# Optimization experiments

Hardware: AMD Instinct MI355X
Metric: run time of the kernel (lower is better)

## Reference

```python
import jax, jax.numpy as jnp
import numpy as np

NUM_HEADS = 12
DIM = 768
HW = 64                # h = w = 64, seqlen = 4096
L = HW * HW
HIDDEN = 4 * DIM


def _dwconv(img, w, b):
    # img: (C, H, W); w: (C, 1, 3, 3) depthwise; b: (C,)
    y = jax.lax.conv_general_dilated(
        img[None], w, window_strides=(1, 1), padding=((1, 1), (1, 1)),
        feature_group_count=img.shape[0],
        dimension_numbers=('NCHW', 'OIHW', 'NCHW'))[0]
    return y + b[:, None, None]


def _ln(t, w, b, eps=1e-5):
    mu = t.mean(-1, keepdims=True)
    var = ((t - mu) ** 2).mean(-1, keepdims=True)
    return (t - mu) / jnp.sqrt(var + eps) * w + b


def _rope_cos_sin(H, W, D, base=10000.0):
    # MLLA-style axial 2D RoPE over feature dim D: k_max = D // (2*ndim)
    k_max = D // 4
    theta = 1.0 / (base ** (jnp.arange(k_max, dtype=jnp.float32) / k_max))
    ax = jnp.arange(H, dtype=jnp.float32)[:, None, None] * theta  # (H,1,k)
    ay = jnp.arange(W, dtype=jnp.float32)[None, :, None] * theta  # (1,W,k)
    angles = jnp.concatenate([
        jnp.broadcast_to(ax, (H, W, k_max)),
        jnp.broadcast_to(ay, (H, W, k_max))], axis=-1)  # (H, W, D/2)
    return jnp.cos(angles), jnp.sin(angles)


def _rope_apply(t, cos, sin):
    # t: (H, W, D); rotate consecutive feature pairs (complex mult)
    H, W, D = t.shape
    t2 = t.reshape(H, W, D // 2, 2)
    x0, x1 = t2[..., 0], t2[..., 1]
    return jnp.stack([x0 * cos - x1 * sin, x0 * sin + x1 * cos], axis=-1).reshape(H, W, D)


def setup_inputs() -> dict:
    key = jax.random.key(0)
    ks = jax.random.split(key, 18)
    s = 0.02
    f32 = jnp.float32
    return {
        'x': jax.random.normal(ks[0], (L, DIM), f32),
        'cpe1_w': jax.random.normal(ks[1], (DIM, 1, 3, 3), f32) * s,
        'cpe1_b': jnp.zeros((DIM,), f32),
        'norm1_w': jnp.ones((DIM,), f32),
        'norm1_b': jnp.zeros((DIM,), f32),
        'qk_w': jax.random.normal(ks[2], (2 * DIM, DIM), f32) * s,
        'qk_b': jnp.zeros((2 * DIM,), f32),
        'lepe_w': jax.random.normal(ks[3], (DIM, 1, 3, 3), f32) * s,
        'lepe_b': jnp.zeros((DIM,), f32),
        'cpe2_w': jax.random.normal(ks[4], (DIM, 1, 3, 3), f32) * s,
        'cpe2_b': jnp.zeros((DIM,), f32),
        'norm2_w': jnp.ones((DIM,), f32),
        'norm2_b': jnp.zeros((DIM,), f32),
        'fc1_w': jax.random.normal(ks[5], (HIDDEN, DIM), f32) * s,
        'fc1_b': jnp.zeros((HIDDEN,), f32),
        'fc2_w': jax.random.normal(ks[6], (DIM, HIDDEN), f32) * s,
        'fc2_b': jnp.zeros((DIM,), f32),
    }


def reference(x, cpe1_w, cpe1_b, norm1_w, norm1_b, qk_w, qk_b, lepe_w, lepe_b,
              cpe2_w, cpe2_b, norm2_w, norm2_b, fc1_w, fc1_b, fc2_w, fc2_b):
    n, C = x.shape          # (4096, 768)
    Hh = Ww = HW
    h, d = NUM_HEADS, C // NUM_HEADS

    # --- CPE1 + norm1 ---
    x1 = x + _dwconv(x.T.reshape(C, Hh, Ww), cpe1_w, cpe1_b).reshape(C, n).T
    x1 = _ln(x1, norm1_w, norm1_b)

    # --- LinearAttention (ELU+1 kernel, RoPE, LePE) ---
    qk = x1 @ qk_w.T + qk_b                                   # (n, 2C)
    q = qk[:, :C].reshape(n, h, d).transpose(1, 0, 2)          # (h, n, d)
    k = qk[:, C:].reshape(n, h, d).transpose(1, 0, 2)
    v = x1.reshape(n, h, d).transpose(1, 0, 2)
    q = jax.nn.elu(q) + 1.0
    k = jax.nn.elu(k) + 1.0

    cos, sin = _rope_cos_sin(Hh, Ww, C)
    to2d = lambda t: t.transpose(1, 0, 2).reshape(Hh, Ww, C)
    from2d = lambda t: t.reshape(n, h, d).transpose(1, 0, 2)
    q_rope = from2d(_rope_apply(to2d(q), cos, sin))
    k_rope = from2d(_rope_apply(to2d(k), cos, sin))

    z = 1.0 / (jnp.einsum('hnd,hd->hn', q, k.mean(axis=1)) + 1e-6)
    scale = n ** (-0.5)
    kv = jnp.einsum('hnd,hne->hde', k_rope * scale, v * scale)  # (h, d, d)
    a = jnp.einsum('hnd,hde->hne', q_rope, kv) * z[..., None]   # (h, n, d)
    a = a.transpose(1, 0, 2).reshape(n, C)

    lepe_out = _dwconv(x1.T.reshape(C, Hh, Ww), lepe_w, lepe_b).reshape(C, n).T
    x1 = a + lepe_out

    # --- residual + CPE2 + MLP ---
    x = x + x1
    x = x + _dwconv(x.T.reshape(C, Hh, Ww), cpe2_w, cpe2_b).reshape(C, n).T
    y = _ln(x, norm2_w, norm2_b)
    y = jax.nn.silu(y @ fc1_w.T + fc1_b) @ fc2_w.T + fc2_b
    return x + y
```

## Files before the change

### kernel.cpp

```cpp
#include <hip/hip_runtime.h>
#include <hip/hip_bf16.h>
#include <stdint.h>

#define DIM 768
#define NTOK 4096

typedef __bf16 bf16x8_t __attribute__((ext_vector_type(8)));
typedef float f32x4_t __attribute__((ext_vector_type(4)));
typedef unsigned short u16x8 __attribute__((ext_vector_type(8)));

__device__ __forceinline__ float bf2f(unsigned short u) {
    union { unsigned int i; float f; } v; v.i = ((unsigned int)u) << 16; return v.f;
}
__device__ __forceinline__ unsigned short f2bf(float f) {
    union { float f; unsigned int i; } v; v.f = f;
    unsigned int x = v.i;
    unsigned int r = x + 0x7fffu + ((x >> 16) & 1u);
    return (unsigned short)(r >> 16);
}
__device__ __forceinline__ u16x8 pack8(const float4& a, const float4& b) {
    u16x8 o;
    o[0] = f2bf(a.x); o[1] = f2bf(a.y); o[2] = f2bf(a.z); o[3] = f2bf(a.w);
    o[4] = f2bf(b.x); o[5] = f2bf(b.y); o[6] = f2bf(b.z); o[7] = f2bf(b.w);
    return o;
}

__device__ __forceinline__ void gload_lds16(const void* g, void* l) {
    __builtin_amdgcn_global_load_lds((const __attribute__((address_space(1))) void*)g,
                                     (__attribute__((address_space(3))) void*)l, 16, 0, 0);
}

__global__ __launch_bounds__(256) void prep(
    const float* __restrict__ qkw, const float* __restrict__ fc1w, const float* __restrict__ fc2w,
    unsigned short* __restrict__ oqk, unsigned short* __restrict__ ofc1,
    unsigned short* __restrict__ ofc2, float* __restrict__ zbuf)
{
    const int b = blockIdx.x, t = threadIdx.x;
    const float* src; unsigned short* dst; int rel;
    if (b < 1152)      { src = qkw;  dst = oqk;  rel = b; }
    else if (b < 3456) { src = fc1w; dst = ofc1; rel = b - 1152; }
    else if (b < 5760) { src = fc2w; dst = ofc2; rel = b - 3456; }
    else { zbuf[(b - 5760) * 256 + t] = 0.f; return; }
    int i = rel * 1024 + t * 4;
    float4 v = *(const float4*)&src[i];
    ushort4 o;
    o.x = f2bf(v.x); o.y = f2bf(v.y); o.z = f2bf(v.z); o.w = f2bf(v.w);
    *(ushort4*)&dst[i] = o;
}

template<int DO_LN, int BASE_BF16, int CIN_BF16, int PRE_BF16>
__global__ __launch_bounds__(256) void conv_ln(
    const void* __restrict__ base_, const void* __restrict__ cin_,
    const float* __restrict__ cw, const float* __restrict__ cb,
    const float* __restrict__ lnw, const float* __restrict__ lnb,
    void* __restrict__ pre_out, unsigned short* __restrict__ lnb16_out)
{
    const int n = blockIdx.x;
    const int hh = n >> 6, ww = n & 63;
    const int t = threadIdx.x;
    float s[3];
#pragma unroll
    for (int i = 0; i < 3; i++) {
        int c = t + i * 256;
        float acc = cb[c];
#pragma unroll
        for (int dh = -1; dh <= 1; dh++) {
            int h2 = hh + dh;
            if ((unsigned)h2 < 64u) {
#pragma unroll
                for (int dw = -1; dw <= 1; dw++) {
                    int w2 = ww + dw;
                    if ((unsigned)w2 < 64u) {
                        size_t idx = (size_t)(h2 * 64 + w2) * DIM + c;
                        float cv = CIN_BF16 ? bf2f(((const unsigned short*)cin_)[idx])
                                            : ((const float*)cin_)[idx];
                        acc = fmaf(cv, cw[c * 9 + (dh + 1) * 3 + (dw + 1)], acc);
                    }
                }
            }
        }
        size_t idx = (size_t)n * DIM + c;
        float v = (BASE_BF16 ? bf2f(((const unsigned short*)base_)[idx])
                             : ((const float*)base_)[idx]) + acc;
        s[i] = v;
        if (pre_out) {
            if (PRE_BF16) ((unsigned short*)pre_out)[idx] = f2bf(v);
            else          ((float*)pre_out)[idx] = v;
        }
    }
    if (DO_LN) {
        float s1 = s[0] + s[1] + s[2];
        float s2 = s[0] * s[0] + s[1] * s[1] + s[2] * s[2];
#pragma unroll
        for (int o = 32; o; o >>= 1) { s1 += __shfl_xor(s1, o); s2 += __shfl_xor(s2, o); }
        __shared__ float red[8];
        int w = t >> 6, lane = t & 63;
        if (lane == 0) { red[w * 2] = s1; red[w * 2 + 1] = s2; }
        __syncthreads();
        s1 = red[0] + red[2] + red[4] + red[6];
        s2 = red[1] + red[3] + red[5] + red[7];
        float mean = s1 * (1.f / 768.f);
        float var = s2 * (1.f / 768.f) - mean * mean;
        float rstd = rsqrtf(var + 1e-5f);
#pragma unroll
        for (int i = 0; i < 3; i++) {
            int c = t + i * 256;
            float vn = (s[i] - mean) * rstd * lnw[c] + lnb[c];
            lnb16_out[(size_t)n * DIM + c] = f2bf(vn);
        }
    }
}

template<int BM, int NBX, int PR, int PC, int SILU, int OUTBF16, int ADD, int ADDBF16, int ROPE>
__global__ __launch_bounds__(256, 3) void gemm_bt(
    const unsigned short* __restrict__ A, const unsigned short* __restrict__ B,
    const float* __restrict__ bias, const void* __restrict__ addsrc,
    void* __restrict__ outp,
    unsigned short* __restrict__ qr, unsigned short* __restrict__ krs,
    unsigned short* __restrict__ qpre, float* __restrict__ ksum,
    int N, int K)
{
    constexpr int BN  = 64;
    constexpr int RB  = BM / 4;
    constexpr int MF  = RB / 16;
    constexpr int ACW = BM / 32;
    constexpr int BCW = BN / 32;
    constexpr int XC  = NBX / PC;
    __shared__ __align__(128) unsigned short aL[2][BM * 64];
    __shared__ __align__(128) unsigned short bL[2][BN * 64];

    const int xcd = blockIdx.x & 7, local = blockIdx.x >> 3;
    const int brow = (xcd / XC) * PR + local / PC;
    const int bcol = (xcd % XC) * PC + local % PC;
    const int t = threadIdx.x, w = t >> 6, lane = t & 63;
    const int lr = lane >> 3;
    const int sl = (lane & 7) ^ lr;

    const unsigned short* aSrc[ACW];
#pragma unroll
    for (int i = 0; i < ACW; i++)
        aSrc[i] = A + (size_t)(brow * BM + (w * ACW + i) * 8 + lr) * K + sl * 8;
    const unsigned short* bSrc[BCW];
#pragma unroll
    for (int i = 0; i < BCW; i++)
        bSrc[i] = B + (size_t)(bcol * BN + (w * BCW + i) * 8 + lr) * K + sl * 8;

    f32x4_t acc[MF][4];
#pragma unroll
    for (int m = 0; m < MF; m++)
#pragma unroll
        for (int n = 0; n < 4; n++) acc[m][n] = (f32x4_t){0.f, 0.f, 0.f, 0.f};

#define STAGE(buf, k0) do { \
    _Pragma("unroll") for (int i_ = 0; i_ < ACW; i_++) \
        gload_lds16(aSrc[i_] + (k0), &aL[buf][(w * ACW + i_) * 512]); \
    _Pragma("unroll") for (int i_ = 0; i_ < BCW; i_++) \
        gload_lds16(bSrc[i_] + (k0), &bL[buf][(w * BCW + i_) * 512]); } while (0)

    const int nt = K >> 6;
    STAGE(0, 0);
    __syncthreads();

    const int fr = lane & 15;
    const int xr = (fr & 7) << 4;
    const int cbase = (lane >> 4) << 4;
    for (int tt = 0; tt < nt; ++tt) {
        if (tt + 1 < nt) STAGE((tt + 1) & 1, (tt + 1) * 64);
        const char* ab = (const char*)aL[tt & 1];
        const char* bb = (const char*)bL[tt & 1];
#pragma unroll
        for (int ks = 0; ks < 2; ks++) {
            bf16x8_t af[MF], bfv[4];
#pragma unroll
            for (int m = 0; m < MF; m++)
                af[m] = *(const bf16x8_t*)(ab + (((w * RB + m * 16 + fr) * 128 + cbase + ks * 64) ^ xr));
#pragma unroll
            for (int n = 0; n < 4; n++)
                bfv[n] = *(const bf16x8_t*)(bb + (((n * 16 + fr) * 128 + cbase + ks * 64) ^ xr));
            __builtin_amdgcn_s_setprio(1);
#pragma unroll
            for (int m = 0; m < MF; m++)
#pragma unroll
                for (int n = 0; n < 4; n++)
                    acc[m][n] = __builtin_amdgcn_mfma_f32_16x16x32_bf16(af[m], bfv[n], acc[m][n], 0, 0, 0);
            __builtin_amdgcn_s_setprio(0);
        }
        __syncthreads();
    }
#undef STAGE

    const int rb = brow * BM + w * RB + (lane >> 4) * 4;
    const int cb = bcol * BN + fr;

    if constexpr (ROPE) {
        const bool isq = (bcol < 12);
        const bool use_h = ((bcol % 12) < 6);
#pragma unroll
        for (int n = 0; n < 4; n++) {
            int col = cb + n * 16;
            float bs = bias[col];
            int cm = isq ? col : col - 768;
            int p = cm >> 1;
            int pmv = use_h ? p : p - 192;
            float th = __expf(-(float)pmv * (9.210340371976184f / 192.f));
            float kssum = 0.f;
#pragma unroll
            for (int m = 0; m < MF; m++) {
#pragma unroll
                for (int j = 0; j < 4; j++) {
                    int row = rb + m * 16 + j;
                    float v = acc[m][n][j] + bs;
                    float e = v > 0.f ? v + 1.f : __expf(v);
                    float pe = __shfl_xor(e, 1);
                    float pos = use_h ? (float)(row >> 6) : (float)(row & 63);
                    float sa, ca;
                    __sincosf(pos * th, &sa, &ca);
                    float rot = (fr & 1) ? (pe * sa + e * ca) : (e * ca - pe * sa);
                    if (isq) {
                        qr[(size_t)row * 768 + col] = f2bf(rot);
                        qpre[(size_t)row * 768 + col] = f2bf(e);
                    } else {
                        krs[(size_t)row * 768 + cm] = f2bf(rot * 0.015625f);
                        kssum += e;
                    }
                }
            }
            if (!isq) {
                kssum += __shfl_xor(kssum, 16);
                kssum += __shfl_xor(kssum, 32);
                if (lane < 16) atomicAdd(&ksum[cm], kssum);
            }
        }
    } else {
#pragma unroll
        for (int n = 0; n < 4; n++) {
            int col = cb + n * 16;
            float bs = bias ? bias[col] : 0.f;
#pragma unroll
            for (int m = 0; m < MF; m++) {
#pragma unroll
                for (int j = 0; j < 4; j++) {
                    int row = rb + m * 16 + j;
                    float v = acc[m][n][j] + bs;
                    if (SILU) v = v / (1.f + __expf(-v));
                    if (ADD) {
                        size_t idx = (size_t)row * N + col;
                        v += ADDBF16 ? bf2f(((const unsigned short*)addsrc)[idx])
                                     : ((const float*)addsrc)[idx];
                    }
                    if (OUTBF16) ((unsigned short*)outp)[(size_t)row * N + col] = f2bf(v);
                    else ((float*)outp)[(size_t)row * N + col] = v;
                }
            }
        }
    }
}

__global__ __launch_bounds__(256) void kv_accum(
    const unsigned short* __restrict__ krs, const unsigned short* __restrict__ x1b,
    float* __restrict__ kvout)
{
    const int chunk = blockIdx.x, h = blockIdx.y;
    const int n0 = chunk * 128;
    __shared__ float kl[128][64];
    __shared__ float vl[128][64];
    const int t = threadIdx.x;
    const int r = t >> 1, cs = (t & 1) * 32;
#pragma unroll
    for (int j = 0; j < 32; j += 8) {
        u16x8 kk = *(const u16x8*)&krs[(size_t)(n0 + r) * DIM + h * 64 + cs + j];
        u16x8 vv = *(const u16x8*)&x1b[(size_t)(n0 + r) * DIM + h * 64 + cs + j];
#pragma unroll
        for (int e = 0; e < 8; e++) {
            kl[r][cs + j + e] = bf2f(kk[e]);
            vl[r][cs + j + e] = bf2f(vv[e]) * 0.015625f;
        }
    }
    __syncthreads();
    const int td = t >> 4, te = t & 15;
    float a[4][4] = {};
    for (int nn = 0; nn < 128; nn++) {
        f32x4_t kd = *(const f32x4_t*)&kl[nn][td * 4];
        f32x4_t ve = *(const f32x4_t*)&vl[nn][te * 4];
#pragma unroll
        for (int i = 0; i < 4; i++)
#pragma unroll
            for (int j = 0; j < 4; j++)
                a[i][j] = fmaf(kd[i], ve[j], a[i][j]);
    }
#pragma unroll
    for (int i = 0; i < 4; i++)
#pragma unroll
        for (int j = 0; j < 4; j++)
            atomicAdd(&kvout[h * 4096 + (te * 4 + j) * 64 + (td * 4 + i)], a[i][j]);
}

__global__ __launch_bounds__(256) void attn_lepe(
    const unsigned short* __restrict__ qr, const unsigned short* __restrict__ qpre,
    const float* __restrict__ ksum, const float* __restrict__ kvT,
    const float* __restrict__ x, const unsigned short* __restrict__ x1b,
    const float* __restrict__ lepe_w, const float* __restrict__ lepe_b,
    unsigned short* __restrict__ x2b)
{
    const int h = blockIdx.y;
    const int chunk = blockIdx.x;
    const int n0 = chunk * 128;
    const int c0 = h * 64;
    const int R0 = chunk * 2;
    const int t = threadIdx.x, w = t >> 6, lane = t & 63;
    __shared__ __align__(128) unsigned short kvL[64 * 64];
    __shared__ __align__(128) unsigned short x1L[4][64][64];
    __shared__ float zl[128];
    __shared__ float kmL[64];

    {
        const int e = t >> 2, db = (t & 3) * 16;
        const float* src = &kvT[h * 4096 + e * 64 + db];
        float4 v0 = *(const float4*)&src[0];
        float4 v1 = *(const float4*)&src[4];
        float4 v2 = *(const float4*)&src[8];
        float4 v3 = *(const float4*)&src[12];
        int s0 = ((db >> 3) + 0) ^ (e & 7);
        int s1 = ((db >> 3) + 1) ^ (e & 7);
        *(u16x8*)((char*)kvL + e * 128 + s0 * 16) = pack8(v0, v1);
        *(u16x8*)((char*)kvL + e * 128 + s1 * 16) = pack8(v2, v3);
    }
    {
        const int r = t >> 6, ww = t & 63;
        const int rr = R0 - 1 + r;
        const bool ok = (unsigned)rr < 64u;
        const unsigned short* sp = &x1b[(size_t)(rr * 64 + ww) * DIM + c0];
#pragma unroll
        for (int jj = 0; jj < 8; jj++) {
            u16x8 vv;
            if (ok) vv = *(const u16x8*)(sp + jj * 8);
            else    vv = (u16x8)(0);
            *(u16x8*)&x1L[r][ww][jj * 8] = vv;
        }
    }
    if (t < 64) kmL[t] = ksum[h * 64 + t] * (1.f / 4096.f);
    __syncthreads();

    {
        const int tok = t >> 1, half = (t & 1) * 32;
        const unsigned short* qp = &qpre[(size_t)(n0 + tok) * DIM + c0 + half];
        float zs = 0.f;
#pragma unroll
        for (int j = 0; j < 32; j += 8) {
            u16x8 qv = *(const u16x8*)&qp[j];
#pragma unroll
            for (int e = 0; e < 8; e++) zs = fmaf(bf2f(qv[e]), kmL[half + j + e], zs);
        }
        zs += __shfl_xor(zs, 1);
        if ((t & 1) == 0) zl[tok] = 1.f / (zs + 1e-6f);
    }
    __syncthreads();

    const int fr = lane & 15;
    const int kc = (lane >> 4) * 8;
    const unsigned short* qbase = qr + (size_t)(n0 + w * 32 + fr) * DIM + c0 + kc;

    f32x4_t acc[2][4];
#pragma unroll
    for (int m = 0; m < 2; m++)
#pragma unroll
        for (int n = 0; n < 4; n++) acc[m][n] = (f32x4_t){0.f, 0.f, 0.f, 0.f};

#pragma unroll
    for (int ks = 0; ks < 2; ks++) {
        bf16x8_t af[2], bfv[4];
#pragma unroll
        for (int m = 0; m < 2; m++)
            af[m] = *(const bf16x8_t*)(qbase + (size_t)m * 16 * DIM + ks * 32);
#pragma unroll
        for (int n = 0; n < 4; n++) {
            int e = n * 16 + fr;
            int slot = (ks * 4 + (lane >> 4)) ^ (e & 7);
            bfv[n] = *(const bf16x8_t*)((const char*)kvL + e * 128 + slot * 16);
        }
#pragma unroll
        for (int m = 0; m < 2; m++)
#pragma unroll
            for (int n = 0; n < 4; n++)
                acc[m][n] = __builtin_amdgcn_mfma_f32_16x16x32_bf16(af[m], bfv[n], acc[m][n], 0, 0, 0);
    }

    const int r4 = (lane >> 4) * 4;
#pragma unroll
    for (int n = 0; n < 4; n++) {
        const int cc = n * 16 + fr;
        const int c = c0 + cc;
        float w9[9];
#pragma unroll
        for (int q2 = 0; q2 < 9; q2++) w9[q2] = lepe_w[c * 9 + q2];
        const float lb = lepe_b[c];
#pragma unroll
        for (int m = 0; m < 2; m++) {
#pragma unroll
            for (int j = 0; j < 4; j++) {
                const int tr = w * 32 + m * 16 + r4 + j;
                float av = acc[m][n][j] * zl[tr];
                const int ww = tr & 63;
                const int rbase = (tr >> 6) + 1;
                float conv = 0.f;
#pragma unroll
                for (int dh = -1; dh <= 1; dh++) {
#pragma unroll
                    for (int dw = -1; dw <= 1; dw++) {
                        int w2 = ww + dw;
                        if ((unsigned)w2 < 64u)
                            conv = fmaf(bf2f(x1L[rbase + dh][w2][cc]),
                                        w9[(dh + 1) * 3 + (dw + 1)], conv);
                    }
                }
                float xr2 = x[(size_t)(n0 + tr) * DIM + c];
                x2b[(size_t)(n0 + tr) * DIM + c] = f2bf(xr2 + av + conv + lb);
            }
        }
    }
}

extern "C" void kernel_launch(void* const* d_in, const int* in_sizes, int n_in,
                              void* d_out, int out_size, void* d_ws, size_t ws_size,
                              hipStream_t stream) {
    (void)in_sizes; (void)n_in; (void)out_size; (void)ws_size;
    const float* x       = (const float*)d_in[0];
    const float* cpe1_w  = (const float*)d_in[1];
    const float* cpe1_b  = (const float*)d_in[2];
    const float* norm1_w = (const float*)d_in[3];
    const float* norm1_b = (const float*)d_in[4];
    const float* qk_w    = (const float*)d_in[5];
    const float* qk_b    = (const float*)d_in[6];
    const float* lepe_w  = (const float*)d_in[7];
    const float* lepe_b  = (const float*)d_in[8];
    const float* cpe2_w  = (const float*)d_in[9];
    const float* cpe2_b  = (const float*)d_in[10];
    const float* norm2_w = (const float*)d_in[11];
    const float* norm2_b = (const float*)d_in[12];
    const float* fc1_w   = (const float*)d_in[13];
    const float* fc1_b   = (const float*)d_in[14];
    const float* fc2_w   = (const float*)d_in[15];
    const float* fc2_b   = (const float*)d_in[16];
    char* ws = (char*)d_ws;

    constexpr size_t o_qkwb  = 0;
    constexpr size_t o_fc1wb = o_qkwb  + (size_t)1536 * 768 * 2;
    constexpr size_t o_fc2wb = o_fc1wb + (size_t)3072 * 768 * 2;
    constexpr size_t o_x1b   = o_fc2wb + (size_t)768 * 3072 * 2;
    constexpr size_t o_big   = o_x1b   + (size_t)4096 * 768 * 2;
    constexpr size_t o_qr    = o_big   + (size_t)4096 * 3072 * 2;
    constexpr size_t o_krs   = o_qr    + (size_t)4096 * 768 * 2;
    constexpr size_t o_qpre  = o_krs   + (size_t)4096 * 768 * 2;
    constexpr size_t o_ksum  = o_qpre  + (size_t)4096 * 768 * 2;
    constexpr size_t o_kv    = o_ksum  + (size_t)768 * 4;
    constexpr size_t o_x3b   = o_kv    + (size_t)12 * 64 * 64 * 4;
    constexpr size_t o_yb    = o_x3b   + (size_t)4096 * 768 * 2;

    unsigned short* x2b = (unsigned short*)(ws + o_big);
    unsigned short* h_b = (unsigned short*)(ws + o_big);

    prep<<<5955, 256, 0, stream>>>(qk_w, fc1_w, fc2_w,
                                   (unsigned short*)(ws + o_qkwb), (unsigned short*)(ws + o_fc1wb),
                                   (unsigned short*)(ws + o_fc2wb), (float*)(ws + o_ksum));
    conv_ln<1, 0, 0, 0><<<4096, 256, 0, stream>>>(x, x, cpe1_w, cpe1_b, norm1_w, norm1_b,
                                                  nullptr, (unsigned short*)(ws + o_x1b));
    gemm_bt<128, 24, 8, 12, 0, 0, 0, 0, 1><<<768, 256, 0, stream>>>(
        (const unsigned short*)(ws + o_x1b), (const unsigned short*)(ws + o_qkwb),
        qk_b, nullptr, nullptr,
        (unsigned short*)(ws + o_qr), (unsigned short*)(ws + o_krs),
        (unsigned short*)(ws + o_qpre), (float*)(ws + o_ksum),
        1536, 768);
    kv_accum<<<dim3(32, 12), 256, 0, stream>>>((const unsigned short*)(ws + o_krs),
                                               (const unsigned short*)(ws + o_x1b),
                                               (float*)(ws + o_kv));
    attn_lepe<<<dim3(32, 12), 256, 0, stream>>>((const unsigned short*)(ws + o_qr),
                                                (const unsigned short*)(ws + o_qpre),
                                                (const float*)(ws + o_ksum), (const float*)(ws + o_kv),
                                                x, (const unsigned short*)(ws + o_x1b),
                                                lepe_w, lepe_b, x2b);
    conv_ln<1, 1, 1, 1><<<4096, 256, 0, stream>>>(x2b, x2b, cpe2_w, cpe2_b, norm2_w, norm2_b,
                                                  (void*)(ws + o_x3b), (unsigned short*)(ws + o_yb));
    gemm_bt<128, 48, 16, 12, 1, 1, 0, 0, 0><<<1536, 256, 0, stream>>>(
        (const unsigned short*)(ws + o_yb), (const unsigned short*)(ws + o_fc1wb),
        fc1_b, nullptr, h_b, nullptr, nullptr, nullptr, nullptr,
        3072, 768);
    gemm_bt<128, 12, 8, 6, 0, 0, 1, 1, 0><<<384, 256, 0, stream>>>(
        h_b, (const unsigned short*)(ws + o_fc2wb),
        fc2_b, (const void*)(ws + o_x3b), d_out, nullptr, nullptr, nullptr, nullptr,
        768, 3072);
}
```

Baseline: 205.7 us.

## Replace LDS-staged GEMM with direct global-to-register double-buffered 128x128 tiles

Rewrites the bf16 GEMM to load MFMA fragments directly from global memory into registers with two-stage register double buffering, removing LDS staging and barriers. Tiles become 128x128 with each of four waves computing a 64x64 subtile, and grids are halved accordingly. This cuts LDS and sync overhead but loses shared reuse across waves, increases L2 traffic with uncoalesced 16-byte row loads, and reduces block count below the CU count for some GEMMs.

```diff
diff --git a/kernel.cpp b/kernel.cpp
--- a/kernel.cpp
+++ b/kernel.cpp
@@ -23,11 +23,6 @@
     o[0] = f2bf(a.x); o[1] = f2bf(a.y); o[2] = f2bf(a.z); o[3] = f2bf(a.w);
     o[4] = f2bf(b.x); o[5] = f2bf(b.y); o[6] = f2bf(b.z); o[7] = f2bf(b.w);
     return o;
-}
-
-__device__ __forceinline__ void gload_lds16(const void* g, void* l) {
-    __builtin_amdgcn_global_load_lds((const __attribute__((address_space(1))) void*)g,
-                                     (__attribute__((address_space(3))) void*)l, 16, 0, 0);
 }
 
 __global__ __launch_bounds__(256) void prep(
@@ -111,8 +106,8 @@
     }
 }
 
-template<int BM, int NBX, int PR, int PC, int SILU, int OUTBF16, int ADD, int ADDBF16, int ROPE>
-__global__ __launch_bounds__(256, 3) void gemm_bt(
+template<int NBX, int PR, int PC, int SILU, int OUTBF16, int ADD, int ADDBF16, int ROPE>
+__global__ __launch_bounds__(256, 2) void gemm_nb(
     const unsigned short* __restrict__ A, const unsigned short* __restrict__ B,
     const float* __restrict__ bias, const void* __restrict__ addsrc,
     void* __restrict__ outp,
@@ -120,81 +115,59 @@
     unsigned short* __restrict__ qpre, float* __restrict__ ksum,
     int N, int K)
 {
-    constexpr int BN  = 64;
-    constexpr int RB  = BM / 4;
-    constexpr int MF  = RB / 16;
-    constexpr int ACW = BM / 32;
-    constexpr int BCW = BN / 32;
-    constexpr int XC  = NBX / PC;
-    __shared__ __align__(128) unsigned short aL[2][BM * 64];
-    __shared__ __align__(128) unsigned short bL[2][BN * 64];
-
+    constexpr int XC = NBX / PC;
     const int xcd = blockIdx.x & 7, local = blockIdx.x >> 3;
     const int brow = (xcd / XC) * PR + local / PC;
     const int bcol = (xcd % XC) * PC + local % PC;
     const int t = threadIdx.x, w = t >> 6, lane = t & 63;
-    const int lr = lane >> 3;
-    const int sl = (lane & 7) ^ lr;
-
-    const unsigned short* aSrc[ACW];
-#pragma unroll
-    for (int i = 0; i < ACW; i++)
-        aSrc[i] = A + (size_t)(brow * BM + (w * ACW + i) * 8 + lr) * K + sl * 8;
-    const unsigned short* bSrc[BCW];
-#pragma unroll
-    for (int i = 0; i < BCW; i++)
-        bSrc[i] = B + (size_t)(bcol * BN + (w * BCW + i) * 8 + lr) * K + sl * 8;
-
-    f32x4_t acc[MF][4];
-#pragma unroll
-    for (int m = 0; m < MF; m++)
+    const int wr = w >> 1, wc = w & 1;
+    const int fr = lane & 15;
+    const int kc = (lane >> 4) * 8;
+
+    const unsigned short* pa[4];
+#pragma unroll
+    for (int m = 0; m < 4; m++)
+        pa[m] = A + (size_t)(brow * 128 + wr * 64 + m * 16 + fr) * K + kc;
+    const unsigned short* pb[4];
+#pragma unroll
+    for (int n = 0; n < 4; n++)
+        pb[n] = B + (size_t)(bcol * 128 + wc * 64 + n * 16 + fr) * K + kc;
+
+    f32x4_t acc[4][4];
+#pragma unroll
+    for (int m = 0; m < 4; m++)
 #pragma unroll
         for (int n = 0; n < 4; n++) acc[m][n] = (f32x4_t){0.f, 0.f, 0.f, 0.f};
 
-#define STAGE(buf, k0) do { \
-    _Pragma("unroll") for (int i_ = 0; i_ < ACW; i_++) \
-        gload_lds16(aSrc[i_] + (k0), &aL[buf][(w * ACW + i_) * 512]); \
-    _Pragma("unroll") for (int i_ = 0; i_ < BCW; i_++) \
-        gload_lds16(bSrc[i_] + (k0), &bL[buf][(w * BCW + i_) * 512]); } while (0)
-
-    const int nt = K >> 6;
-    STAGE(0, 0);
-    __syncthreads();
-
-    const int fr = lane & 15;
-    const int xr = (fr & 7) << 4;
-    const int cbase = (lane >> 4) << 4;
-    for (int tt = 0; tt < nt; ++tt) {
-        if (tt + 1 < nt) STAGE((tt + 1) & 1, (tt + 1) * 64);
-        const char* ab = (const char*)aL[tt & 1];
-        const char* bb = (const char*)bL[tt & 1];
-#pragma unroll
-        for (int ks = 0; ks < 2; ks++) {
-            bf16x8_t af[MF], bfv[4];
-#pragma unroll
-            for (int m = 0; m < MF; m++)
-                af[m] = *(const bf16x8_t*)(ab + (((w * RB + m * 16 + fr) * 128 + cbase + ks * 64) ^ xr));
-#pragma unroll
-            for (int n = 0; n < 4; n++)
-                bfv[n] = *(const bf16x8_t*)(bb + (((n * 16 + fr) * 128 + cbase + ks * 64) ^ xr));
-            __builtin_amdgcn_s_setprio(1);
-#pragma unroll
-            for (int m = 0; m < MF; m++)
-#pragma unroll
-                for (int n = 0; n < 4; n++)
-                    acc[m][n] = __builtin_amdgcn_mfma_f32_16x16x32_bf16(af[m], bfv[n], acc[m][n], 0, 0, 0);
-            __builtin_amdgcn_s_setprio(0);
-        }
-        __syncthreads();
-    }
-#undef STAGE
-
-    const int rb = brow * BM + w * RB + (lane >> 4) * 4;
-    const int cb = bcol * BN + fr;
+    bf16x8_t fa[2][4], fb[2][4];
+#define LOADS(s, kof) do { \
+    _Pragma("unroll") for (int m_ = 0; m_ < 4; m_++) fa[s][m_] = *(const bf16x8_t*)(pa[m_] + (kof)); \
+    _Pragma("unroll") for (int n_ = 0; n_ < 4; n_++) fb[s][n_] = *(const bf16x8_t*)(pb[n_] + (kof)); } while (0)
+#define MM(s) do { \
+    __builtin_amdgcn_s_setprio(1); \
+    _Pragma("unroll") for (int m_ = 0; m_ < 4; m_++) \
+        _Pragma("unroll") for (int n_ = 0; n_ < 4; n_++) \
+            acc[m_][n_] = __builtin_amdgcn_mfma_f32_16x16x32_bf16(fa[s][m_], fb[s][n_], acc[m_][n_], 0, 0, 0); \
+    __builtin_amdgcn_s_setprio(0); } while (0)
+
+    const int nt = K >> 5;
+    LOADS(0, 0);
+    LOADS(1, 32);
+    for (int kk = 0; kk < nt; kk += 2) {
+        MM(0);
+        if (kk + 2 < nt) LOADS(0, (kk + 2) * 32);
+        MM(1);
+        if (kk + 3 < nt) LOADS(1, (kk + 3) * 32);
+    }
+#undef LOADS
+#undef MM
+
+    const int rb = brow * 128 + wr * 64 + (lane >> 4) * 4;
+    const int cb = bcol * 128 + wc * 64 + fr;
 
     if constexpr (ROPE) {
-        const bool isq = (bcol < 12);
-        const bool use_h = ((bcol % 12) < 6);
+        const bool isq = (bcol < 6);
+        const bool use_h = ((bcol % 6) < 3);
 #pragma unroll
         for (int n = 0; n < 4; n++) {
             int col = cb + n * 16;
@@ -205,7 +178,7 @@
             float th = __expf(-(float)pmv * (9.210340371976184f / 192.f));
             float kssum = 0.f;
 #pragma unroll
-            for (int m = 0; m < MF; m++) {
+            for (int m = 0; m < 4; m++) {
 #pragma unroll
                 for (int j = 0; j < 4; j++) {
                     int row = rb + m * 16 + j;
@@ -237,7 +210,7 @@
             int col = cb + n * 16;
             float bs = bias ? bias[col] : 0.f;
 #pragma unroll
-            for (int m = 0; m < MF; m++) {
+            for (int m = 0; m < 4; m++) {
 #pragma unroll
                 for (int j = 0; j < 4; j++) {
                     int row = rb + m * 16 + j;
@@ -464,7 +437,7 @@
                                    (unsigned short*)(ws + o_fc2wb), (float*)(ws + o_ksum));
     conv_ln<1, 0, 0, 0><<<4096, 256, 0, stream>>>(x, x, cpe1_w, cpe1_b, norm1_w, norm1_b,
                                                   nullptr, (unsigned short*)(ws + o_x1b));
-    gemm_bt<128, 24, 8, 12, 0, 0, 0, 0, 1><<<768, 256, 0, stream>>>(
+    gemm_nb<12, 8, 6, 0, 0, 0, 0, 1><<<384, 256, 0, stream>>>(
         (const unsigned short*)(ws + o_x1b), (const unsigned short*)(ws + o_qkwb),
         qk_b, nullptr, nullptr,
         (unsigned short*)(ws + o_qr), (unsigned short*)(ws + o_krs),
@@ -480,11 +453,11 @@
                                                 lepe_w, lepe_b, x2b);
     conv_ln<1, 1, 1, 1><<<4096, 256, 0, stream>>>(x2b, x2b, cpe2_w, cpe2_b, norm2_w, norm2_b,
                                                   (void*)(ws + o_x3b), (unsigned short*)(ws + o_yb));
-    gemm_bt<128, 48, 16, 12, 1, 1, 0, 0, 0><<<1536, 256, 0, stream>>>(
+    gemm_nb<24, 8, 12, 1, 1, 0, 0, 0><<<768, 256, 0, stream>>>(
         (const unsigned short*)(ws + o_yb), (const unsigned short*)(ws + o_fc1wb),
         fc1_b, nullptr, h_b, nullptr, nullptr, nullptr, nullptr,
         3072, 768);
-    gemm_bt<128, 12, 8, 6, 0, 0, 1, 1, 0><<<384, 256, 0, stream>>>(
+    gemm_nb<6, 4, 6, 0, 0, 1, 1, 0><<<192, 256, 0, stream>>>(
         h_b, (const unsigned short*)(ws + o_fc2wb),
         fc2_b, (const void*)(ws + o_x3b), d_out, nullptr, nullptr, nullptr, nullptr,
         768, 3072);
```

Measured after the change: 325.9 us. 1.58x slower.
